# Kernel tuning notes

Measured on AMD Instinct MI355X. Metric: run time of the kernel, lower is better.

Reference implementation:

```python
import jax, jax.numpy as jnp
import numpy as np

B, L, D, NC, H = 2, 192, 768, 4, 256  # batch, seq_len, bert_hidden, num_case(+coref), hidden


def setup_inputs() -> dict:
    key = jax.random.key(0)
    ks = jax.random.split(key, 9)
    s = 0.02  # init scale
    return {
        "sequence_output": jax.random.normal(ks[0], (B, L, D), dtype=jnp.float32),
        "base_score": jax.random.normal(ks[1], (B, L, NC, L), dtype=jnp.float32),
        "Wp": jax.random.normal(ks[2], (D, H), dtype=jnp.float32) * s,
        "bp": jnp.zeros((H,), dtype=jnp.float32),
        "Wa": jax.random.normal(ks[3], (D, NC * H), dtype=jnp.float32) * s,
        "ba": jnp.zeros((NC * H,), dtype=jnp.float32),
        "Wmid": jax.random.normal(ks[4], (NC, H + NC, H), dtype=jnp.float32) * s,
        "bmid": jnp.zeros((NC, H), dtype=jnp.float32),
        "Wout": jax.random.normal(ks[5], (NC, H), dtype=jnp.float32) * s,
    }


def reference(sequence_output, base_score, Wp, bp, Wa, ba, Wmid, bmid, Wout):
    b, l, d = sequence_output.shape
    nc = Wmid.shape[0]
    h = Wp.shape[1]
    # dropout is identity in eval mode
    h_p = sequence_output @ Wp + bp                       # [B, L, H] (predicate)
    h_a = (sequence_output @ Wa + ba).reshape(b, l, nc, h)  # [B, L, NC, H] (argument)
    # broadcast add: predicate axis p, argument axis a -> [B, P, A, NC, H]
    h_pa = jnp.tanh(h_p[:, :, None, None, :] + h_a[:, None, :, :, :])
    # base_score [B, L, NC, L] -> transpose(2,3) -> [B, P, A, NC], expand over case axis
    bs = jnp.swapaxes(base_score, 2, 3)                   # [B, P, A, NC]
    bs = jnp.broadcast_to(bs[:, :, :, None, :], (b, l, l, nc, nc))
    hcat = jnp.concatenate([h_pa, bs], axis=-1)           # [B, P, A, NC, H+NC]
    # per-case mid Linear, batched as a single einsum over the case axis n
    h_mid = jnp.tanh(jnp.einsum('bpanc,nch->bpanh', hcat, Wmid) + bmid)
    out = jnp.einsum('bpanh,nh->bpan', h_mid, Wout)       # [B, P, A, NC]
    return jnp.transpose(out, (0, 1, 3, 2))               # [B, P, NC, A]
```

## Files before the change

kernel.cpp:

```cpp
#include <hip/hip_runtime.h>

#define LSEQ 192
#define DIM  768
#define NCASE 4
#define HID  256
#define BATCH 2

#define TANH_K 2.885390081777927f

typedef float  floatx4 __attribute__((ext_vector_type(4)));
typedef __bf16 bf16x8  __attribute__((ext_vector_type(8)));

__device__ __forceinline__ float tanh_pre(float x) {
    float e = __builtin_amdgcn_exp2f(x);
    return 1.0f - 2.0f * __builtin_amdgcn_rcpf(e + 1.0f);
}

__device__ __forceinline__ void barrier_lds_only() {
    __builtin_amdgcn_sched_barrier(0);
    __builtin_amdgcn_s_waitcnt(0xC07F);
    __builtin_amdgcn_s_barrier();
    __builtin_amdgcn_sched_barrier(0);
}

template <int CTRL>
__device__ __forceinline__ float dpp_add(float v) {
    int x = __builtin_amdgcn_update_dpp(0, __builtin_bit_cast(int, v),
                                        CTRL, 0xF, 0xF, true);
    return v + __builtin_bit_cast(float, x);
}
__device__ __forceinline__ float row16_reduce(float v) {
    v = dpp_add<0xB1>(v);
    v = dpp_add<0x4E>(v);
    v = dpp_add<0x141>(v);
    v = dpp_add<0x140>(v);
    return v;
}


__global__ __launch_bounds__(256) void prep(
    const float* __restrict__ seq, const float* __restrict__ Wp,
    const float* __restrict__ Wa,  const float* __restrict__ bp,
    const float* __restrict__ ba,  const float* __restrict__ Wmid,
    const float* __restrict__ bmid,
    float* __restrict__ lin, bf16x8* __restrict__ Bpack)
{
    const int blk = blockIdx.x;
    const int tid = threadIdx.x;

    if (blk >= 480) {
        int u = (blk - 480) * 256 + tid;
        int lane = u & 63, f = u >> 6;
        int ct = f & 15, nk = f >> 4;
        int kc = nk % 9, n = nk / 9;
        int h = ct * 16 + (lane & 15);
        int kbase = kc * 32 + ((lane >> 4) & 3) * 8;
        bf16x8 v;
        #pragma unroll
        for (int j = 0; j < 8; j++) {
            int k = kbase + j;
            float x;
            if (k < 260)       x = Wmid[(size_t)(n * 260 + k) * 256 + h];
            else if (k == 260) x = bmid[n * 256 + h];
            else               x = 0.0f;
            v[j] = (__bf16)(TANH_K * x);
        }
        Bpack[u] = v;
        return;
    }

    const int w = tid >> 6, lane = tid & 63;
    const int u = blk * 4 + w;
    const int rt = u / 80, cg = u % 80;
    const int quad  = lane >> 4;
    const int col16 = lane & 15;

    const int arow = rt * 16 + col16;
    const int col  = cg * 16 + col16;
    const float* aptr = seq + (size_t)arow * DIM + quad * 8;
    const float* wbase = (cg < 16) ? (Wp + col) : (Wa + (col - 256));
    const int    wstr  = (cg < 16) ? HID : (NCASE * HID);

    floatx4 acc = {};
    floatx4 a0 = *(const floatx4*)(aptr);
    floatx4 a1 = *(const floatx4*)(aptr + 4);
    float bv[8];
    #pragma unroll
    for (int j = 0; j < 8; j++) bv[j] = wbase[(size_t)(quad * 8 + j) * wstr];

    #pragma unroll
    for (int kc = 0; kc < 24; kc++) {
        bf16x8 ah, al, bh, bl;
        #pragma unroll
        for (int j = 0; j < 4; j++) {
            __bf16 h0 = (__bf16)a0[j];
            ah[j] = h0; al[j] = (__bf16)(a0[j] - (float)h0);
            __bf16 h1 = (__bf16)a1[j];
            ah[4 + j] = h1; al[4 + j] = (__bf16)(a1[j] - (float)h1);
        }
        #pragma unroll
        for (int j = 0; j < 8; j++) {
            __bf16 h = (__bf16)bv[j];
            bh[j] = h; bl[j] = (__bf16)(bv[j] - (float)h);
        }
        if (kc < 23) {
            a0 = *(const floatx4*)(aptr + (kc + 1) * 32);
            a1 = *(const floatx4*)(aptr + (kc + 1) * 32 + 4);
            #pragma unroll
            for (int j = 0; j < 8; j++)
                bv[j] = wbase[(size_t)((kc + 1) * 32 + quad * 8 + j) * wstr];
        }
        acc = __builtin_amdgcn_mfma_f32_16x16x32_bf16(ah, bh, acc, 0, 0, 0);
        acc = __builtin_amdgcn_mfma_f32_16x16x32_bf16(al, bh, acc, 0, 0, 0);
        acc = __builtin_amdgcn_mfma_f32_16x16x32_bf16(ah, bl, acc, 0, 0, 0);
    }
    const float bias = (cg < 16) ? bp[col] : ba[col - 256];
    #pragma unroll
    for (int reg = 0; reg < 4; reg++)
        lin[(size_t)(rt * 16 + quad * 4 + reg) * 1280 + col] =
            TANH_K * (acc[reg] + bias);
}

__global__ __launch_bounds__(256, 2) void refine_main(
    const float* __restrict__ lin,
    const float* __restrict__ base_score,
    const float* __restrict__ Wout,
    const bf16x8* __restrict__ Bpack,
    float* __restrict__ out)
{
    const int bx = blockIdx.x;
    const int n  = blockIdx.y;
    const int b  = blockIdx.z;
    const int ptile = bx / 24, atile = bx % 24;
    const int p0 = ptile * 8, a0 = atile * 8;

    const int tid   = threadIdx.x;
    const int w     = tid >> 6;
    const int lane  = tid & 63;
    const int quad  = lane >> 4;
    const int col16 = lane & 15;

    __shared__ __align__(16) __bf16 A0[256 * 8];
    __shared__ __align__(16) __bf16 A1[256 * 8];
    __shared__ float red[4][64];

    const int row_gen = w * 16 + col16;
    const int pg = p0 + (row_gen >> 3), ag = a0 + (row_gen & 7);
    const float* hp_ptr = lin + (size_t)(b * LSEQ + pg) * 1280 + quad * 8;
    const float* ha_ptr = lin + (size_t)(b * LSEQ + ag) * 1280 + 256 + n * 256 + quad * 8;

    const bf16x8* bbase = Bpack + ((size_t)(n * 9) * 16 + w * 4) * 64 + lane;

    float bs4[4], wo[4];
    #pragma unroll
    for (int j = 0; j < 4; j++)
        bs4[j] = base_score[((size_t)(b * LSEQ + pg) * NCASE + j) * LSEQ + ag];
    #pragma unroll
    for (int ct = 0; ct < 4; ct++)
        wo[ct] = Wout[n * 256 + w * 64 + ct * 16 + col16];

    bf16x8 bcur[4];
    #pragma unroll
    for (int ct = 0; ct < 4; ct++) bcur[ct] = bbase[ct * 64];

    floatx4 hp0 = *(const floatx4*)(hp_ptr);
    floatx4 hp1 = *(const floatx4*)(hp_ptr + 4);
    floatx4 ha0 = *(const floatx4*)(ha_ptr);
    floatx4 ha1 = *(const floatx4*)(ha_ptr + 4);
    {
        floatx4 s0 = hp0 + ha0, s1 = hp1 + ha1;
        bf16x8 av;
        #pragma unroll
        for (int j = 0; j < 4; j++) {
            av[j]     = (__bf16)tanh_pre(s0[j]);
            av[4 + j] = (__bf16)tanh_pre(s1[j]);
        }
        *(bf16x8*)&A0[tid * 8] = av;
    }
    hp0 = *(const floatx4*)(hp_ptr + 32);
    hp1 = *(const floatx4*)(hp_ptr + 36);
    ha0 = *(const floatx4*)(ha_ptr + 32);
    ha1 = *(const floatx4*)(ha_ptr + 36);
    barrier_lds_only();

    floatx4 acc[4][4] = {};

    #pragma unroll
    for (int kc = 0; kc < 9; kc++) {
        bf16x8 bnext[4];
        if (kc < 8) {
            #pragma unroll
            for (int ct = 0; ct < 4; ct++)
                bnext[ct] = bbase[((kc + 1) * 16 + ct) * 64];
        }
        if (kc < 7) {
            floatx4 s0 = hp0 + ha0, s1 = hp1 + ha1;
            if (kc < 6) {
                hp0 = *(const floatx4*)(hp_ptr + (kc + 2) * 32);
                hp1 = *(const floatx4*)(hp_ptr + (kc + 2) * 32 + 4);
                ha0 = *(const floatx4*)(ha_ptr + (kc + 2) * 32);
                ha1 = *(const floatx4*)(ha_ptr + (kc + 2) * 32 + 4);
            }
            bf16x8 av;
            #pragma unroll
            for (int j = 0; j < 4; j++) {
                av[j]     = (__bf16)tanh_pre(s0[j]);
                av[4 + j] = (__bf16)tanh_pre(s1[j]);
            }
            __bf16* buf = ((kc + 1) & 1) ? A1 : A0;
            *(bf16x8*)&buf[tid * 8] = av;
        } else if (kc == 7) {
            bf16x8 av = {};
            if (quad == 0) {
                #pragma unroll
                for (int j = 0; j < 4; j++) av[j] = (__bf16)bs4[j];
                av[4] = (__bf16)1.0f;
            }
            *(bf16x8*)&A0[tid * 8] = av;
        }

        const __bf16* rb = (kc & 1) ? A1 : A0;
        bf16x8 af[4];
        #pragma unroll
        for (int rt = 0; rt < 4; rt++)
            af[rt] = *(const bf16x8*)&rb[(rt * 64 + lane) * 8];
        #pragma unroll
        for (int rt = 0; rt < 4; rt++)
            #pragma unroll
            for (int ct = 0; ct < 4; ct++)
                acc[rt][ct] = __builtin_amdgcn_mfma_f32_16x16x32_bf16(
                    af[rt], bcur[ct], acc[rt][ct], 0, 0, 0);
        #pragma unroll
        for (int ct = 0; ct < 4; ct++) bcur[ct] = bnext[ct];
        if (kc < 8) barrier_lds_only();
    }

    #pragma unroll
    for (int rt = 0; rt < 4; rt++) {
        #pragma unroll
        for (int reg = 0; reg < 4; reg++) {
            float rs = 0.0f;
            #pragma unroll
            for (int ct = 0; ct < 4; ct++)
                rs += tanh_pre(acc[rt][ct][reg]) * wo[ct];
            rs = row16_reduce(rs);
            if (col16 == 0) red[w][rt * 16 + quad * 4 + reg] = rs;
        }
    }
    barrier_lds_only();

    if (tid < 64) {
        float total = red[0][tid] + red[1][tid] + red[2][tid] + red[3][tid];
        const int p = p0 + (tid >> 3), a = a0 + (tid & 7);
        out[((size_t)(b * LSEQ + p) * NCASE + n) * LSEQ + a] = total;
    }
}

extern "C" void kernel_launch(void* const* d_in, const int* in_sizes, int n_in,
                              void* d_out, int out_size, void* d_ws, size_t ws_size,
                              hipStream_t stream) {
    const float* seq  = (const float*)d_in[0];
    const float* bsc  = (const float*)d_in[1];
    const float* Wp   = (const float*)d_in[2];
    const float* bp   = (const float*)d_in[3];
    const float* Wa   = (const float*)d_in[4];
    const float* ba   = (const float*)d_in[5];
    const float* Wmid = (const float*)d_in[6];
    const float* bmid = (const float*)d_in[7];
    const float* Wout = (const float*)d_in[8];
    float* out = (float*)d_out;

    char* ws = (char*)d_ws;
    float*  lin   = (float*)(ws);
    bf16x8* Bpack = (bf16x8*)(ws + 1966080);

    prep<<<624, 256, 0, stream>>>(seq, Wp, Wa, bp, ba, Wmid, bmid, lin, Bpack);
    refine_main<<<dim3(576, NCASE, BATCH), 256, 0, stream>>>(
        lin, bsc, Wout, Bpack, out);
}
```

Before: 151.8 us.

## Process two K-chunks per barrier phase and swap tanh for Pade approximant

Restructures the main loop so each barrier phase builds and consumes two 32-wide K-chunks, which halves the number of LDS barriers, and adds a separate buffer for the final base-score/bias chunk. The exp2+rcp tanh is replaced by a clamped rational Pade approximation, and the TANH_K prescaling is removed from the weight pack and from the linear stage. The aim is less synchronisation and cheaper transcendental work, at the cost of more registers, twice the LDS, and reduced tanh accuracy for larger inputs.

```diff
diff --git a/kernel.cpp b/kernel.cpp
--- a/kernel.cpp
+++ b/kernel.cpp
@@ -6,14 +6,15 @@
 #define HID  256
 #define BATCH 2
 
-#define TANH_K 2.885390081777927f
-
 typedef float  floatx4 __attribute__((ext_vector_type(4)));
 typedef __bf16 bf16x8  __attribute__((ext_vector_type(8)));
 
-__device__ __forceinline__ float tanh_pre(float x) {
-    float e = __builtin_amdgcn_exp2f(x);
-    return 1.0f - 2.0f * __builtin_amdgcn_rcpf(e + 1.0f);
+__device__ __forceinline__ float tanh_pade(float x) {
+    float x2 = x * x;
+    float num = x * (945.0f + x2 * (105.0f + x2));
+    float den = 945.0f + x2 * (420.0f + x2 * 15.0f);
+    float r = num * __builtin_amdgcn_rcpf(den);
+    return __builtin_fminf(1.0f, __builtin_fmaxf(-1.0f, r));
 }
 
 __device__ __forceinline__ void barrier_lds_only() {
@@ -63,7 +64,7 @@
             if (k < 260)       x = Wmid[(size_t)(n * 260 + k) * 256 + h];
             else if (k == 260) x = bmid[n * 256 + h];
             else               x = 0.0f;
-            v[j] = (__bf16)(TANH_K * x);
+            v[j] = (__bf16)x;
         }
         Bpack[u] = v;
         return;
@@ -117,8 +118,7 @@
     const float bias = (cg < 16) ? bp[col] : ba[col - 256];
     #pragma unroll
     for (int reg = 0; reg < 4; reg++)
-        lin[(size_t)(rt * 16 + quad * 4 + reg) * 1280 + col] =
-            TANH_K * (acc[reg] + bias);
+        lin[(size_t)(rt * 16 + quad * 4 + reg) * 1280 + col] = acc[reg] + bias;
 }
 
 __global__ __launch_bounds__(256, 2) void refine_main(
@@ -132,7 +132,7 @@
     const int n  = blockIdx.y;
     const int b  = blockIdx.z;
     const int ptile = bx / 24, atile = bx % 24;
-    const int p0 = ptile * 8, a0 = atile * 8;
+    const int p0 = ptile * 8, a0r = atile * 8;
 
     const int tid   = threadIdx.x;
     const int w     = tid >> 6;
@@ -140,12 +140,12 @@
     const int quad  = lane >> 4;
     const int col16 = lane & 15;
 
-    __shared__ __align__(16) __bf16 A0[256 * 8];
-    __shared__ __align__(16) __bf16 A1[256 * 8];
+    __shared__ __align__(16) __bf16 Abuf[2][2 * 2048];
+    __shared__ __align__(16) __bf16 Afold[2048];
     __shared__ float red[4][64];
 
     const int row_gen = w * 16 + col16;
-    const int pg = p0 + (row_gen >> 3), ag = a0 + (row_gen & 7);
+    const int pg = p0 + (row_gen >> 3), ag = a0r + (row_gen & 7);
     const float* hp_ptr = lin + (size_t)(b * LSEQ + pg) * 1280 + quad * 8;
     const float* ha_ptr = lin + (size_t)(b * LSEQ + ag) * 1280 + 256 + n * 256 + quad * 8;
 
@@ -159,80 +159,109 @@
     for (int ct = 0; ct < 4; ct++)
         wo[ct] = Wout[n * 256 + w * 64 + ct * 16 + col16];
 
-    bf16x8 bcur[4];
-    #pragma unroll
-    for (int ct = 0; ct < 4; ct++) bcur[ct] = bbase[ct * 64];
-
-    floatx4 hp0 = *(const floatx4*)(hp_ptr);
-    floatx4 hp1 = *(const floatx4*)(hp_ptr + 4);
-    floatx4 ha0 = *(const floatx4*)(ha_ptr);
-    floatx4 ha1 = *(const floatx4*)(ha_ptr + 4);
+    floatx4 hpA0, hpA1, haA0, haA1, hpB0, hpB1, haB0, haB1;
+    hpA0 = *(const floatx4*)(hp_ptr);       hpA1 = *(const floatx4*)(hp_ptr + 4);
+    haA0 = *(const floatx4*)(ha_ptr);       haA1 = *(const floatx4*)(ha_ptr + 4);
+    hpB0 = *(const floatx4*)(hp_ptr + 32);  hpB1 = *(const floatx4*)(hp_ptr + 36);
+    haB0 = *(const floatx4*)(ha_ptr + 32);  haB1 = *(const floatx4*)(ha_ptr + 36);
     {
-        floatx4 s0 = hp0 + ha0, s1 = hp1 + ha1;
-        bf16x8 av;
+        floatx4 s0 = hpA0 + haA0, s1 = hpA1 + haA1;
+        floatx4 t0 = hpB0 + haB0, t1 = hpB1 + haB1;
+        bf16x8 av, bv2;
         #pragma unroll
         for (int j = 0; j < 4; j++) {
-            av[j]     = (__bf16)tanh_pre(s0[j]);
-            av[4 + j] = (__bf16)tanh_pre(s1[j]);
-        }
-        *(bf16x8*)&A0[tid * 8] = av;
-    }
-    hp0 = *(const floatx4*)(hp_ptr + 32);
-    hp1 = *(const floatx4*)(hp_ptr + 36);
-    ha0 = *(const floatx4*)(ha_ptr + 32);
-    ha1 = *(const floatx4*)(ha_ptr + 36);
+            av[j]      = (__bf16)tanh_pade(s0[j]);
+            av[4 + j]  = (__bf16)tanh_pade(s1[j]);
+            bv2[j]     = (__bf16)tanh_pade(t0[j]);
+            bv2[4 + j] = (__bf16)tanh_pade(t1[j]);
+        }
+        *(bf16x8*)&Abuf[0][tid * 8] = av;
+        *(bf16x8*)&Abuf[0][2048 + tid * 8] = bv2;
+    }
+    hpA0 = *(const floatx4*)(hp_ptr + 64);  hpA1 = *(const floatx4*)(hp_ptr + 68);
+    haA0 = *(const floatx4*)(ha_ptr + 64);  haA1 = *(const floatx4*)(ha_ptr + 68);
+    hpB0 = *(const floatx4*)(hp_ptr + 96);  hpB1 = *(const floatx4*)(hp_ptr + 100);
+    haB0 = *(const floatx4*)(ha_ptr + 96);  haB1 = *(const floatx4*)(ha_ptr + 100);
     barrier_lds_only();
 
     floatx4 acc[4][4] = {};
 
     #pragma unroll
-    for (int kc = 0; kc < 9; kc++) {
-        bf16x8 bnext[4];
-        if (kc < 8) {
-            #pragma unroll
-            for (int ct = 0; ct < 4; ct++)
-                bnext[ct] = bbase[((kc + 1) * 16 + ct) * 64];
-        }
-        if (kc < 7) {
-            floatx4 s0 = hp0 + ha0, s1 = hp1 + ha1;
-            if (kc < 6) {
-                hp0 = *(const floatx4*)(hp_ptr + (kc + 2) * 32);
-                hp1 = *(const floatx4*)(hp_ptr + (kc + 2) * 32 + 4);
-                ha0 = *(const floatx4*)(ha_ptr + (kc + 2) * 32);
-                ha1 = *(const floatx4*)(ha_ptr + (kc + 2) * 32 + 4);
+    for (int ph = 0; ph < 4; ph++) {
+        bf16x8 b0[4], b1[4];
+        #pragma unroll
+        for (int ct = 0; ct < 4; ct++) {
+            b0[ct] = bbase[((2 * ph) * 16 + ct) * 64];
+            b1[ct] = bbase[((2 * ph + 1) * 16 + ct) * 64];
+        }
+
+        if (ph < 3) {
+            floatx4 s0 = hpA0 + haA0, s1 = hpA1 + haA1;
+            floatx4 t0 = hpB0 + haB0, t1 = hpB1 + haB1;
+            if (ph < 2) {
+                hpA0 = *(const floatx4*)(hp_ptr + (2 * ph + 4) * 32);
+                hpA1 = *(const floatx4*)(hp_ptr + (2 * ph + 4) * 32 + 4);
+                haA0 = *(const floatx4*)(ha_ptr + (2 * ph + 4) * 32);
+                haA1 = *(const floatx4*)(ha_ptr + (2 * ph + 4) * 32 + 4);
+                hpB0 = *(const floatx4*)(hp_ptr + (2 * ph + 5) * 32);
+                hpB1 = *(const floatx4*)(hp_ptr + (2 * ph + 5) * 32 + 4);
+                haB0 = *(const floatx4*)(ha_ptr + (2 * ph + 5) * 32);
+                haB1 = *(const floatx4*)(ha_ptr + (2 * ph + 5) * 32 + 4);
             }
-            bf16x8 av;
+            bf16x8 av, bv2;
             #pragma unroll
             for (int j = 0; j < 4; j++) {
-                av[j]     = (__bf16)tanh_pre(s0[j]);
-                av[4 + j] = (__bf16)tanh_pre(s1[j]);
+                av[j]      = (__bf16)tanh_pade(s0[j]);
+                av[4 + j]  = (__bf16)tanh_pade(s1[j]);
+                bv2[j]     = (__bf16)tanh_pade(t0[j]);
+                bv2[4 + j] = (__bf16)tanh_pade(t1[j]);
             }
-            __bf16* buf = ((kc + 1) & 1) ? A1 : A0;
+            __bf16* buf = Abuf[(ph + 1) & 1];
             *(bf16x8*)&buf[tid * 8] = av;
-        } else if (kc == 7) {
+            *(bf16x8*)&buf[2048 + tid * 8] = bv2;
+        } else {
             bf16x8 av = {};
             if (quad == 0) {
                 #pragma unroll
                 for (int j = 0; j < 4; j++) av[j] = (__bf16)bs4[j];
                 av[4] = (__bf16)1.0f;
             }
-            *(bf16x8*)&A0[tid * 8] = av;
-        }
-
-        const __bf16* rb = (kc & 1) ? A1 : A0;
+            *(bf16x8*)&Afold[tid * 8] = av;
+        }
+
+        const __bf16* rb = Abuf[ph & 1];
+        bf16x8 af0[4], af1[4];
+        #pragma unroll
+        for (int rt = 0; rt < 4; rt++) {
+            af0[rt] = *(const bf16x8*)&rb[(rt * 64 + lane) * 8];
+            af1[rt] = *(const bf16x8*)&rb[2048 + (rt * 64 + lane) * 8];
+        }
+        #pragma unroll
+        for (int rt = 0; rt < 4; rt++)
+            #pragma unroll
+            for (int ct = 0; ct < 4; ct++) {
+                acc[rt][ct] = __builtin_amdgcn_mfma_f32_16x16x32_bf16(
+                    af0[rt], b0[ct], acc[rt][ct], 0, 0, 0);
+                acc[rt][ct] = __builtin_amdgcn_mfma_f32_16x16x32_bf16(
+                    af1[rt], b1[ct], acc[rt][ct], 0, 0, 0);
+            }
+        barrier_lds_only();
+    }
+
+    {
+        bf16x8 bf[4];
+        #pragma unroll
+        for (int ct = 0; ct < 4; ct++) bf[ct] = bbase[(8 * 16 + ct) * 64];
         bf16x8 af[4];
         #pragma unroll
         for (int rt = 0; rt < 4; rt++)
-            af[rt] = *(const bf16x8*)&rb[(rt * 64 + lane) * 8];
+            af[rt] = *(const bf16x8*)&Afold[(rt * 64 + lane) * 8];
         #pragma unroll
         for (int rt = 0; rt < 4; rt++)
             #pragma unroll
             for (int ct = 0; ct < 4; ct++)
                 acc[rt][ct] = __builtin_amdgcn_mfma_f32_16x16x32_bf16(
-                    af[rt], bcur[ct], acc[rt][ct], 0, 0, 0);
-        #pragma unroll
-        for (int ct = 0; ct < 4; ct++) bcur[ct] = bnext[ct];
-        if (kc < 8) barrier_lds_only();
+                    af[rt], bf[ct], acc[rt][ct], 0, 0, 0);
     }
 
     #pragma unroll
@@ -242,7 +271,7 @@
             float rs = 0.0f;
             #pragma unroll
             for (int ct = 0; ct < 4; ct++)
-                rs += tanh_pre(acc[rt][ct][reg]) * wo[ct];
+                rs += tanh_pade(acc[rt][ct][reg]) * wo[ct];
             rs = row16_reduce(rs);
             if (col16 == 0) red[w][rt * 16 + quad * 4 + reg] = rs;
         }
@@ -251,7 +280,7 @@
 
     if (tid < 64) {
         float total = red[0][tid] + red[1][tid] + red[2][tid] + red[3][tid];
-        const int p = p0 + (tid >> 3), a = a0 + (tid & 7);
+        const int p = p0 + (tid >> 3), a = a0r + (tid & 7);
         out[((size_t)(b * LSEQ + p) * NCASE + n) * LSEQ + a] = total;
     }
 }
```

Result: slower. 181.3 us (+19.5%).

## Precompute tanh of projections and combine via tanh addition identity

Applied to the files above, without the earlier changes.

The projection kernel now stores tanh of the scaled projections, and the main kernel forms tanh(u+v) as (tu+tv)/(1+tu*tv). This swaps a per-element exp2 plus reciprocal for an FMA and a reciprocal in the hot broadcast loop. The change also keeps each wave's own A fragment in registers, so it skips one of the four LDS reads per k-chunk. The identity is exact in maths but rounds slightly differently, and it relies on the conversion to bf16 to keep the error small.

```diff
diff --git a/kernel.cpp b/kernel.cpp
--- a/kernel.cpp
+++ b/kernel.cpp
@@ -14,6 +14,11 @@
 __device__ __forceinline__ float tanh_pre(float x) {
     float e = __builtin_amdgcn_exp2f(x);
     return 1.0f - 2.0f * __builtin_amdgcn_rcpf(e + 1.0f);
+}
+
+__device__ __forceinline__ float tanh_add(float tu, float tv) {
+    float den = __builtin_fmaf(tu, tv, 1.0f);
+    return (tu + tv) * __builtin_amdgcn_rcpf(den);
 }
 
 __device__ __forceinline__ void barrier_lds_only() {
@@ -118,7 +123,7 @@
     #pragma unroll
     for (int reg = 0; reg < 4; reg++)
         lin[(size_t)(rt * 16 + quad * 4 + reg) * 1280 + col] =
-            TANH_K * (acc[reg] + bias);
+            tanh_pre(TANH_K * (acc[reg] + bias));
 }
 
 __global__ __launch_bounds__(256, 2) void refine_main(
@@ -132,7 +137,7 @@
     const int n  = blockIdx.y;
     const int b  = blockIdx.z;
     const int ptile = bx / 24, atile = bx % 24;
-    const int p0 = ptile * 8, a0 = atile * 8;
+    const int p0 = ptile * 8, a0r = atile * 8;
 
     const int tid   = threadIdx.x;
     const int w     = tid >> 6;
@@ -145,7 +150,7 @@
     __shared__ float red[4][64];
 
     const int row_gen = w * 16 + col16;
-    const int pg = p0 + (row_gen >> 3), ag = a0 + (row_gen & 7);
+    const int pg = p0 + (row_gen >> 3), ag = a0r + (row_gen & 7);
     const float* hp_ptr = lin + (size_t)(b * LSEQ + pg) * 1280 + quad * 8;
     const float* ha_ptr = lin + (size_t)(b * LSEQ + ag) * 1280 + 256 + n * 256 + quad * 8;
 
@@ -167,15 +172,14 @@
     floatx4 hp1 = *(const floatx4*)(hp_ptr + 4);
     floatx4 ha0 = *(const floatx4*)(ha_ptr);
     floatx4 ha1 = *(const floatx4*)(ha_ptr + 4);
+    bf16x8 av_cur;
     {
-        floatx4 s0 = hp0 + ha0, s1 = hp1 + ha1;
-        bf16x8 av;
         #pragma unroll
         for (int j = 0; j < 4; j++) {
-            av[j]     = (__bf16)tanh_pre(s0[j]);
-            av[4 + j] = (__bf16)tanh_pre(s1[j]);
-        }
-        *(bf16x8*)&A0[tid * 8] = av;
+            av_cur[j]     = (__bf16)tanh_add(hp0[j], ha0[j]);
+            av_cur[4 + j] = (__bf16)tanh_add(hp1[j], ha1[j]);
+        }
+        *(bf16x8*)&A0[tid * 8] = av_cur;
     }
     hp0 = *(const floatx4*)(hp_ptr + 32);
     hp1 = *(const floatx4*)(hp_ptr + 36);
@@ -193,37 +197,45 @@
             for (int ct = 0; ct < 4; ct++)
                 bnext[ct] = bbase[((kc + 1) * 16 + ct) * 64];
         }
+        bf16x8 av_next;
         if (kc < 7) {
-            floatx4 s0 = hp0 + ha0, s1 = hp1 + ha1;
             if (kc < 6) {
+                floatx4 u0 = hp0, u1 = hp1, v0 = ha0, v1 = ha1;
                 hp0 = *(const floatx4*)(hp_ptr + (kc + 2) * 32);
                 hp1 = *(const floatx4*)(hp_ptr + (kc + 2) * 32 + 4);
                 ha0 = *(const floatx4*)(ha_ptr + (kc + 2) * 32);
                 ha1 = *(const floatx4*)(ha_ptr + (kc + 2) * 32 + 4);
-            }
-            bf16x8 av;
-            #pragma unroll
-            for (int j = 0; j < 4; j++) {
-                av[j]     = (__bf16)tanh_pre(s0[j]);
-                av[4 + j] = (__bf16)tanh_pre(s1[j]);
+                #pragma unroll
+                for (int j = 0; j < 4; j++) {
+                    av_next[j]     = (__bf16)tanh_add(u0[j], v0[j]);
+                    av_next[4 + j] = (__bf16)tanh_add(u1[j], v1[j]);
+                }
+            } else {
+                #pragma unroll
+                for (int j = 0; j < 4; j++) {
+                    av_next[j]     = (__bf16)tanh_add(hp0[j], ha0[j]);
+                    av_next[4 + j] = (__bf16)tanh_add(hp1[j], ha1[j]);
+                }
             }
             __bf16* buf = ((kc + 1) & 1) ? A1 : A0;
-            *(bf16x8*)&buf[tid * 8] = av;
+            *(bf16x8*)&buf[tid * 8] = av_next;
         } else if (kc == 7) {
-            bf16x8 av = {};
+            av_next = bf16x8{};
             if (quad == 0) {
                 #pragma unroll
-                for (int j = 0; j < 4; j++) av[j] = (__bf16)bs4[j];
-                av[4] = (__bf16)1.0f;
+                for (int j = 0; j < 4; j++) av_next[j] = (__bf16)bs4[j];
+                av_next[4] = (__bf16)1.0f;
             }
-            *(bf16x8*)&A0[tid * 8] = av;
+            *(bf16x8*)&A0[tid * 8] = av_next;
         }
 
         const __bf16* rb = (kc & 1) ? A1 : A0;
         bf16x8 af[4];
         #pragma unroll
-        for (int rt = 0; rt < 4; rt++)
-            af[rt] = *(const bf16x8*)&rb[(rt * 64 + lane) * 8];
+        for (int rt = 0; rt < 4; rt++) {
+            if (rt == w) af[rt] = av_cur;
+            else         af[rt] = *(const bf16x8*)&rb[(rt * 64 + lane) * 8];
+        }
         #pragma unroll
         for (int rt = 0; rt < 4; rt++)
             #pragma unroll
@@ -232,7 +244,7 @@
                     af[rt], bcur[ct], acc[rt][ct], 0, 0, 0);
         #pragma unroll
         for (int ct = 0; ct < 4; ct++) bcur[ct] = bnext[ct];
-        if (kc < 8) barrier_lds_only();
+        if (kc < 8) { av_cur = av_next; barrier_lds_only(); }
     }
 
     #pragma unroll
@@ -251,7 +263,7 @@
 
     if (tid < 64) {
         float total = red[0][tid] + red[1][tid] + red[2][tid] + red[3][tid];
-        const int p = p0 + (tid >> 3), a = a0 + (tid & 7);
+        const int p = p0 + (tid >> 3), a = a0r + (tid & 7);
         out[((size_t)(b * LSEQ + p) * NCASE + n) * LSEQ + a] = total;
     }
 }
```

Result: no change. 153.5 us (+1.1%).

## Precompute tanh of linear projections and use tanh addition identity; widen blocks to 512

Applied to the files above, without the earlier changes.

The prep kernel now stores tanh of the predicate and argument projections. The main kernel forms tanh(u+v) through the identity (tu+tv)/(1+tu*tv), which replaces one exp2 plus one rcp per pair element with an fma plus one rcp. The main kernel also doubles its threads to 512 (8 waves), with each wave covering 2 column tiles instead of 4. Each thread builds half as many A elements per stage, and the cross-wave reduction grows to 8 partials. This is meant to cut transcendental work in the dominant pairwise stage and raise the number of waves per block, at the cost of a little precision and more reduction overhead.

```diff
diff --git a/kernel.cpp b/kernel.cpp
--- a/kernel.cpp
+++ b/kernel.cpp
@@ -10,10 +10,16 @@
 
 typedef float  floatx4 __attribute__((ext_vector_type(4)));
 typedef __bf16 bf16x8  __attribute__((ext_vector_type(8)));
+typedef __bf16 bf16x4  __attribute__((ext_vector_type(4)));
 
 __device__ __forceinline__ float tanh_pre(float x) {
     float e = __builtin_amdgcn_exp2f(x);
     return 1.0f - 2.0f * __builtin_amdgcn_rcpf(e + 1.0f);
+}
+
+__device__ __forceinline__ float tanh_add(float tu, float tv) {
+    float den = __builtin_fmaf(tu, tv, 1.0f);
+    return (tu + tv) * __builtin_amdgcn_rcpf(den);
 }
 
 __device__ __forceinline__ void barrier_lds_only() {
@@ -118,10 +124,10 @@
     #pragma unroll
     for (int reg = 0; reg < 4; reg++)
         lin[(size_t)(rt * 16 + quad * 4 + reg) * 1280 + col] =
-            TANH_K * (acc[reg] + bias);
-}
-
-__global__ __launch_bounds__(256, 2) void refine_main(
+            tanh_pre(TANH_K * (acc[reg] + bias));
+}
+
+__global__ __launch_bounds__(512, 4) void refine_main(
     const float* __restrict__ lin,
     const float* __restrict__ base_score,
     const float* __restrict__ Wout,
@@ -132,7 +138,7 @@
     const int n  = blockIdx.y;
     const int b  = blockIdx.z;
     const int ptile = bx / 24, atile = bx % 24;
-    const int p0 = ptile * 8, a0 = atile * 8;
+    const int p0 = ptile * 8, a0r = atile * 8;
 
     const int tid   = threadIdx.x;
     const int w     = tid >> 6;
@@ -142,81 +148,80 @@
 
     __shared__ __align__(16) __bf16 A0[256 * 8];
     __shared__ __align__(16) __bf16 A1[256 * 8];
-    __shared__ float red[4][64];
-
-    const int row_gen = w * 16 + col16;
-    const int pg = p0 + (row_gen >> 3), ag = a0 + (row_gen & 7);
-    const float* hp_ptr = lin + (size_t)(b * LSEQ + pg) * 1280 + quad * 8;
-    const float* ha_ptr = lin + (size_t)(b * LSEQ + ag) * 1280 + 256 + n * 256 + quad * 8;
-
-    const bf16x8* bbase = Bpack + ((size_t)(n * 9) * 16 + w * 4) * 64 + lane;
-
-    float bs4[4], wo[4];
-    #pragma unroll
-    for (int j = 0; j < 4; j++)
-        bs4[j] = base_score[((size_t)(b * LSEQ + pg) * NCASE + j) * LSEQ + ag];
-    #pragma unroll
-    for (int ct = 0; ct < 4; ct++)
-        wo[ct] = Wout[n * 256 + w * 64 + ct * 16 + col16];
-
-    bf16x8 bcur[4];
-    #pragma unroll
-    for (int ct = 0; ct < 4; ct++) bcur[ct] = bbase[ct * 64];
-
-    floatx4 hp0 = *(const floatx4*)(hp_ptr);
-    floatx4 hp1 = *(const floatx4*)(hp_ptr + 4);
-    floatx4 ha0 = *(const floatx4*)(ha_ptr);
-    floatx4 ha1 = *(const floatx4*)(ha_ptr + 4);
+    __shared__ float red[8][64];
+
+    const int s_g    = tid >> 1;
+    const int h2     = tid & 1;
+    const int l_g    = s_g & 63;
+    const int m_gen  = ((s_g >> 6) << 4) + (l_g & 15);
+    const int kq     = (l_g >> 4) * 8 + h2 * 4;
+    const int quad_g = l_g >> 4;
+
+    const int pg = p0 + (m_gen >> 3), ag = a0r + (m_gen & 7);
+    const float* hp_ptr = lin + (size_t)(b * LSEQ + pg) * 1280 + kq;
+    const float* ha_ptr = lin + (size_t)(b * LSEQ + ag) * 1280 + 256 + n * 256 + kq;
+
+    const bf16x8* bbase = Bpack + ((size_t)(n * 9) * 16 + w * 2) * 64 + lane;
+
+    float bs4[4] = {};
+    if (quad_g == 0 && h2 == 0) {
+        #pragma unroll
+        for (int j = 0; j < 4; j++)
+            bs4[j] = base_score[((size_t)(b * LSEQ + pg) * NCASE + j) * LSEQ + ag];
+    }
+    float wo[2];
+    #pragma unroll
+    for (int ct = 0; ct < 2; ct++)
+        wo[ct] = Wout[n * 256 + w * 32 + ct * 16 + col16];
+
+    bf16x8 bcur[2];
+    #pragma unroll
+    for (int ct = 0; ct < 2; ct++) bcur[ct] = bbase[ct * 64];
+
+    floatx4 hp = *(const floatx4*)(hp_ptr);
+    floatx4 ha = *(const floatx4*)(ha_ptr);
     {
-        floatx4 s0 = hp0 + ha0, s1 = hp1 + ha1;
-        bf16x8 av;
-        #pragma unroll
-        for (int j = 0; j < 4; j++) {
-            av[j]     = (__bf16)tanh_pre(s0[j]);
-            av[4 + j] = (__bf16)tanh_pre(s1[j]);
-        }
-        *(bf16x8*)&A0[tid * 8] = av;
-    }
-    hp0 = *(const floatx4*)(hp_ptr + 32);
-    hp1 = *(const floatx4*)(hp_ptr + 36);
-    ha0 = *(const floatx4*)(ha_ptr + 32);
-    ha1 = *(const floatx4*)(ha_ptr + 36);
+        bf16x4 av;
+        #pragma unroll
+        for (int j = 0; j < 4; j++) av[j] = (__bf16)tanh_add(hp[j], ha[j]);
+        *(bf16x4*)&A0[tid * 4] = av;
+    }
+    hp = *(const floatx4*)(hp_ptr + 32);
+    ha = *(const floatx4*)(ha_ptr + 32);
     barrier_lds_only();
 
-    floatx4 acc[4][4] = {};
+    floatx4 acc[4][2] = {};
 
     #pragma unroll
     for (int kc = 0; kc < 9; kc++) {
-        bf16x8 bnext[4];
+        bf16x8 bnext[2];
         if (kc < 8) {
             #pragma unroll
-            for (int ct = 0; ct < 4; ct++)
+            for (int ct = 0; ct < 2; ct++)
                 bnext[ct] = bbase[((kc + 1) * 16 + ct) * 64];
         }
         if (kc < 7) {
-            floatx4 s0 = hp0 + ha0, s1 = hp1 + ha1;
+            floatx4 u0 = hp, v0 = ha;
             if (kc < 6) {
-                hp0 = *(const floatx4*)(hp_ptr + (kc + 2) * 32);
-                hp1 = *(const floatx4*)(hp_ptr + (kc + 2) * 32 + 4);
-                ha0 = *(const floatx4*)(ha_ptr + (kc + 2) * 32);
-                ha1 = *(const floatx4*)(ha_ptr + (kc + 2) * 32 + 4);
+                hp = *(const floatx4*)(hp_ptr + (kc + 2) * 32);
+                ha = *(const floatx4*)(ha_ptr + (kc + 2) * 32);
             }
-            bf16x8 av;
-            #pragma unroll
-            for (int j = 0; j < 4; j++) {
-                av[j]     = (__bf16)tanh_pre(s0[j]);
-                av[4 + j] = (__bf16)tanh_pre(s1[j]);
+            bf16x4 av;
+            #pragma unroll
+            for (int j = 0; j < 4; j++) av[j] = (__bf16)tanh_add(u0[j], v0[j]);
+            __bf16* buf = ((kc + 1) & 1) ? A1 : A0;
+            *(bf16x4*)&buf[tid * 4] = av;
+        } else if (kc == 7) {
+            bf16x4 av = {};
+            if (quad_g == 0) {
+                if (h2 == 0) {
+                    #pragma unroll
+                    for (int j = 0; j < 4; j++) av[j] = (__bf16)bs4[j];
+                } else {
+                    av[0] = (__bf16)1.0f;
+                }
             }
-            __bf16* buf = ((kc + 1) & 1) ? A1 : A0;
-            *(bf16x8*)&buf[tid * 8] = av;
-        } else if (kc == 7) {
-            bf16x8 av = {};
-            if (quad == 0) {
-                #pragma unroll
-                for (int j = 0; j < 4; j++) av[j] = (__bf16)bs4[j];
-                av[4] = (__bf16)1.0f;
-            }
-            *(bf16x8*)&A0[tid * 8] = av;
+            *(bf16x4*)&A0[tid * 4] = av;
         }
 
         const __bf16* rb = (kc & 1) ? A1 : A0;
@@ -227,11 +232,11 @@
         #pragma unroll
         for (int rt = 0; rt < 4; rt++)
             #pragma unroll
-            for (int ct = 0; ct < 4; ct++)
+            for (int ct = 0; ct < 2; ct++)
                 acc[rt][ct] = __builtin_amdgcn_mfma_f32_16x16x32_bf16(
                     af[rt], bcur[ct], acc[rt][ct], 0, 0, 0);
         #pragma unroll
-        for (int ct = 0; ct < 4; ct++) bcur[ct] = bnext[ct];
+        for (int ct = 0; ct < 2; ct++) bcur[ct] = bnext[ct];
         if (kc < 8) barrier_lds_only();
     }
 
@@ -239,10 +244,8 @@
     for (int rt = 0; rt < 4; rt++) {
         #pragma unroll
         for (int reg = 0; reg < 4; reg++) {
-            float rs = 0.0f;
-            #pragma unroll
-            for (int ct = 0; ct < 4; ct++)
-                rs += tanh_pre(acc[rt][ct][reg]) * wo[ct];
+            float rs = tanh_pre(acc[rt][0][reg]) * wo[0]
+                     + tanh_pre(acc[rt][1][reg]) * wo[1];
             rs = row16_reduce(rs);
             if (col16 == 0) red[w][rt * 16 + quad * 4 + reg] = rs;
         }
@@ -250,8 +253,9 @@
     barrier_lds_only();
 
     if (tid < 64) {
-        float total = red[0][tid] + red[1][tid] + red[2][tid] + red[3][tid];
-        const int p = p0 + (tid >> 3), a = a0 + (tid & 7);
+        float total = red[0][tid] + red[1][tid] + red[2][tid] + red[3][tid]
+                    + red[4][tid] + red[5][tid] + red[6][tid] + red[7][tid];
+        const int p = p0 + (tid >> 3), a = a0r + (tid & 7);
         out[((size_t)(b * LSEQ + p) * NCASE + n) * LSEQ + a] = total;
     }
 }
@@ -275,6 +279,6 @@
     bf16x8* Bpack = (bf16x8*)(ws + 1966080);
 
     prep<<<624, 256, 0, stream>>>(seq, Wp, Wa, bp, ba, Wmid, bmid, lin, Bpack);
-    refine_main<<<dim3(576, NCASE, BATCH), 256, 0, stream>>>(
+    refine_main<<<dim3(576, NCASE, BATCH), 512, 0, stream>>>(
         lin, bsc, Wout, Bpack, out);
 }
```

Result: no change. 150.5 us (-0.8%).
